# Kernel optimization log

Hardware: AMD Instinct MI355X
Metric: run time of the kernel (lower is better)

The kernel has to match this reference:

```python
import jax, jax.numpy as jnp
import numpy as np

D = 256       # dim
M = 50        # num_celltypes
NPATH = 65536 # path tokens (256*256)
N = M + NPATH
FF = 3        # focusing_factor
K = 5         # dwc kernel size


def find_closest_factors(num):
    for i in range(int(num ** 0.5), 0, -1):
        if num % i == 0:
            return (i, num // i)
    return (1, num)


def setup_inputs() -> dict:
    key = jax.random.key(0)
    ks = jax.random.split(key, 16)
    def w(k, shape, s=0.02):
        return jax.random.normal(k, shape, dtype=jnp.float32) * s
    z = lambda *s: jnp.zeros(s, jnp.float32)
    return {
        "x": jax.random.normal(ks[0], (1, N, D), dtype=jnp.float32),
        "W_qkv": w(ks[1], (D, 3 * D)),
        "scale_linear": w(ks[2], (1, 1, D)),
        "dwc_w": w(ks[3], (D, 1, K, K)),
        "dwc_b": w(ks[4], (D,)),
        "Wa": w(ks[5], (D, D)), "ba": z(D),
        "Wb": w(ks[6], (D, D)), "bb": z(D),
        "Wc": w(ks[7], (D, 1)), "bc": z(1),
        "W1": w(ks[8], (D, D)), "b1": z(D),
        "W2": w(ks[9], (D, D)), "b2": z(D),
        "W3a": w(ks[10], (2 * D, D)), "b3a": z(D),
        "W3b": w(ks[11], (D, D)), "b3b": z(D),
        "Wf": w(ks[12], (D, D)), "bf": z(D),
    }


def reference(x, W_qkv, scale_linear, dwc_w, dwc_b, Wa, ba, Wb, bb, Wc, bc,
              W1, b1, W2, b2, W3a, b3a, W3b, b3b, Wf, bf):
    scale = D ** -0.5
    qkv = x @ W_qkv                         # (1, N, 3D)
    q, k, v = jnp.split(qkv, 3, axis=-1)
    qc, qp = q[:, :M], q[:, M:]
    kc, kp = k[:, :M], k[:, M:]
    vc, vp = v[:, :M], v[:, M:]

    # --- softmax attention branches ---
    sa = jax.nn.softmax(jnp.einsum('bic,bjc->bij', qc * scale, kc), axis=-1)
    out_self_celltypes = sa @ vc            # (1, M, D)
    cap = jax.nn.softmax(jnp.einsum('bic,bjc->bij', qp * scale, kc), axis=-1)
    out_cross_path = cap @ vc               # (1, NPATH, D)
    cac = jax.nn.softmax(jnp.einsum('bic,bjc->bij', qc * scale, kp), axis=-1)
    out_cross_celltypes = cac @ vp          # (1, M, D)

    # --- focused linear attention on path tokens ---
    sp = jax.nn.softplus(scale_linear)
    ql = (jax.nn.relu(qp) + 1e-6) / sp
    kl = (jax.nn.relu(kp) + 1e-6) / sp
    qn = jnp.linalg.norm(ql, axis=-1, keepdims=True)
    kn = jnp.linalg.norm(kl, axis=-1, keepdims=True)
    ql = ql ** FF
    kl = kl ** FF
    ql = ql / jnp.linalg.norm(ql, axis=-1, keepdims=True) * qn
    kl = kl / jnp.linalg.norm(kl, axis=-1, keepdims=True) * kn
    zfac = 1.0 / (jnp.einsum('bic,bc->bi', ql, kl.sum(axis=1)) + 1e-6)
    kv = jnp.einsum('bjc,bjd->bcd', kl, vp)                 # (1, D, D)
    out_s = jnp.einsum('bic,bcd,bi->bid', ql, kv, zfac)     # (1, NPATH, D)

    # --- depthwise conv feature map ---
    wc, hc = find_closest_factors(NPATH)
    fm = vp.reshape(1, wc, hc, D).transpose(0, 3, 1, 2)     # b c w h
    fm = jax.lax.conv_general_dilated(
        fm, dwc_w, (1, 1), 'SAME',
        dimension_numbers=('NCHW', 'OIHW', 'NCHW'), feature_group_count=D)
    fm = fm + dwc_b[None, :, None, None]
    fm = fm.transpose(0, 2, 3, 1).reshape(1, NPATH, D)
    out_self_path = (out_s + fm) @ Wf + bf  # feamap_linear (dropout=eval)

    # --- gated attention net (shared weights, 4 calls) ---
    def gated(t):
        t = t[0]  # squeeze batch -> (n, D)
        a = jnp.tanh(t @ Wa + ba)
        g = jax.nn.sigmoid(t @ Wb + bb)
        return (a * g) @ Wc + bc  # (n, 1)

    A_cc = gated(out_cross_celltypes)
    A_cp = gated(out_cross_path)
    A_sc = gated(out_self_celltypes)
    A_sp = gated(out_self_path)

    # --- attention fusion (shared weights, 2 calls) ---
    def fuse(A1, A2, x1, x2):
        h1 = jax.nn.softmax(A1.T, axis=1) @ x1[0]   # (1, D)
        h1 = jax.nn.relu(h1 @ W1 + b1)
        h2 = jax.nn.softmax(A2.T, axis=1) @ x2[0]
        h2 = jax.nn.relu(h2 @ W2 + b2)
        f = jnp.concatenate([h1, h2], axis=1)       # (1, 2D)
        return jax.nn.relu(jax.nn.relu(f @ W3a + b3a) @ W3b + b3b)

    fusion_cross = fuse(A_cc, A_cp, out_cross_celltypes, out_cross_path)
    fusion_self = fuse(A_sc, A_sp, out_self_celltypes, out_self_path)
    return jnp.concatenate([fusion_cross, fusion_self], axis=1)  # (1, 2D)
```

## Files before the change

kernel.cpp:

```cpp
#include <hip/hip_runtime.h>
#include <hip/hip_bf16.h>
#include <math.h>


constexpr int DD = 256;
constexpr int MM = 50;
constexpr float SCL = 0.0625f;

constexpr size_t B_VPH = 0;
constexpr size_t B_QLH = (size_t)32 << 20;
constexpr size_t B_KLH = (size_t)64 << 20;
constexpr size_t B_E   = (size_t)96 << 20;
constexpr size_t B_SM  = (size_t)112 << 20;
constexpr size_t B_X   = B_SM + ((size_t)2 << 20);

constexpr size_t PP_OFF = (size_t)4 << 20;

constexpr size_t KLSUMR = 0;
constexpr size_t KLSUMP = 256;
constexpr size_t OCCDENP= 2304;
constexpr size_t W50P   = 2816;
constexpr size_t EDENP  = 3328;
constexpr size_t H2TP   = 3336;
constexpr size_t H2DENP = 5384;
constexpr size_t OCCRAW = 5392;
constexpr size_t ZEND   = 18192;
constexpr size_t QC     = ZEND;
constexpr size_t KC     = QC + 12800;
constexpr size_t VC     = KC + 12800;
constexpr size_t VCA    = VC + 12800;
constexpr size_t VCB    = VCA + 12800;
constexpr size_t WFA    = VCB + 12800;
constexpr size_t WFB    = WFA + 65536;
constexpr size_t BFA    = WFB + 65536;
constexpr size_t BFB    = BFA + 256;
constexpr size_t OSCB   = BFB + 256;
constexpr size_t OCCB   = OSCB + 12800;
constexpr size_t ASC    = OCCB + 12800;
constexpr size_t ACC50  = ASC + 64;
constexpr size_t SMEND  = ACC50 + 64;

constexpr size_t XT_WQKV = 0;
constexpr size_t XT_WFAT = 196608;
constexpr size_t XT_WFBT = 262144;
constexpr size_t XT_KVT  = 327680;
constexpr size_t XT_QCH  = 393216;
constexpr size_t XT_KCH  = 409600;
constexpr size_t XT_VCAT = 425984;
constexpr size_t XT_VCBT = 442368;
constexpr size_t XT_END  = 458752;
constexpr size_t WS_NEEDED = B_X + XT_END * 2;

typedef short bf16x8 __attribute__((ext_vector_type(8)));
typedef float f32x4 __attribute__((ext_vector_type(4)));

__device__ __forceinline__ float rcpf_(float x){ return __builtin_amdgcn_rcpf(x); }
__device__ __forceinline__ float fsig_(float x){ return rcpf_(1.0f + __expf(-x)); }
__device__ __forceinline__ float ftanh_(float x){ return 1.0f - 2.0f * rcpf_(__expf(2.0f * x) + 1.0f); }

__device__ __forceinline__ float bf2f(unsigned short u){
  return __uint_as_float(((unsigned int)u) << 16);
}
__device__ __forceinline__ unsigned short f2bf(float f){
  union { __hip_bfloat16 h; unsigned short u; } c;
  c.h = __float2bfloat16(f);
  return c.u;
}
__device__ __forceinline__ f32x4 mfma16(bf16x8 a, bf16x8 b, f32x4 c){
  return __builtin_amdgcn_mfma_f32_16x16x32_bf16(a, b, c, 0, 0, 0);
}

__device__ __forceinline__ float waveAllSum(float v){
  #pragma unroll
  for (int m = 1; m < 64; m <<= 1) v += __shfl_xor(v, m, 64);
  return v;
}

__device__ __forceinline__ size_t fragIdx(int n, int k, int K8){
  const int tile = n >> 4, cn = n & 15;
  const int k0 = k >> 5, kqi = (k >> 3) & 3, e = k & 7;
  return (((size_t)tile * K8 + k0) * 64 + (kqi * 16 + cn)) * 8 + e;
}

__device__ __forceinline__ int kvOff(int c, int k){
  return c * 40 + (c >> 3) * 8 + k;
}

__global__ void __launch_bounds__(256) k_prep0(const float* __restrict__ x, const float* __restrict__ Wqkv,
                                               float* qc, float* kc, float* vc,
                                               unsigned short* qch, unsigned short* kch,
                                               unsigned short* __restrict__ WT,
                                               const float* __restrict__ Wa, const float* __restrict__ Wb,
                                               const float* __restrict__ ba, const float* __restrict__ bb,
                                               const float* __restrict__ Wf, const float* __restrict__ bf,
                                               float* Wfa, float* Wfb, float* bfa, float* bfb,
                                               unsigned short* WfaTh, unsigned short* WfbTh){
  const int b = blockIdx.x, t = threadIdx.x;
  if (b < 48) {
    __shared__ unsigned short Tt[64][72];
    const int bn = b % 12, bk = b / 12;
    const int n0 = bn * 64, k0g = bk * 64;
    #pragma unroll
    for (int i = 0; i < 16; i++) {
      const int k_l = (t >> 6) + i * 4;
      const int n_l = t & 63;
      Tt[n_l][k_l] = f2bf(Wqkv[(size_t)(k0g + k_l) * 768 + n0 + n_l]);
    }
    __syncthreads();
    #pragma unroll
    for (int i = 0; i < 2; i++) {
      const int fr = t * 2 + i;
      const int t_l = fr >> 7;
      const int k0_l = (fr >> 6) & 1;
      const int lane_f = fr & 63;
      const int n_l = t_l * 16 + (lane_f & 15);
      const int k_l = k0_l * 32 + (lane_f >> 4) * 8;
      const int tg = (n0 >> 4) + t_l;
      const int k0gl = (k0g >> 5) + k0_l;
      bf16x8 v = *(const bf16x8*)&Tt[n_l][k_l];
      *(bf16x8*)&WT[(((size_t)tg * 8 + k0gl) * 64 + lane_f) * 8] = v;
    }
    return;
  }
  __shared__ float xs[256];
  const int j = t;
  if (b < 98) {
    const int r = b - 48;
    xs[j] = x[r * DD + j];
    __syncthreads();
    float aq = 0.f, ak = 0.f, av = 0.f;
    for (int k = 0; k < DD; k++) {
      float xv = xs[k];
      aq += xv * Wqkv[k * 768 + j];
      ak += xv * Wqkv[k * 768 + 256 + j];
      av += xv * Wqkv[k * 768 + 512 + j];
    }
    qc[r * DD + j] = aq; kc[r * DD + j] = ak; vc[r * DD + j] = av;
    qch[fragIdx(r, j, 8)] = f2bf(aq);
    kch[fragIdx(r, j, 8)] = f2bf(ak);
    if (r == 0) {
      for (int c = 50; c < 64; c++) {
        qch[fragIdx(c, j, 8)] = 0;
        kch[fragIdx(c, j, 8)] = 0;
      }
    }
    return;
  }
  const int bb2 = b - 98;
  const float* src; const float* Wm;
  if (bb2 < 256)      { src = Wf + bb2 * DD;         Wm = Wa; }
  else if (bb2 < 512) { src = Wf + (bb2 - 256) * DD; Wm = Wb; }
  else if (bb2 == 512){ src = bf;                    Wm = Wa; }
  else                { src = bf;                    Wm = Wb; }
  xs[j] = src[j];
  __syncthreads();
  float a = 0.f;
  for (int k = 0; k < DD; k++) a += xs[k] * Wm[k * DD + j];
  if (bb2 < 256)      { Wfa[bb2 * DD + j] = a; WfaTh[fragIdx(j, bb2, 8)] = f2bf(a); }
  else if (bb2 < 512) { Wfb[(bb2 - 256) * DD + j] = a; WfbTh[fragIdx(j, bb2 - 256, 8)] = f2bf(a); }
  else if (bb2 == 512) bfa[j] = a + ba[j];
  else bfb[j] = a + bb[j];
}

__global__ void __launch_bounds__(256) k_prep1(const float* vc, const float* Wa, const float* Wb,
                                               float* Vca, float* Vcb,
                                               unsigned short* VcaTh, unsigned short* VcbTh){
  __shared__ float rs[256];
  const int b = blockIdx.x, j = threadIdx.x;
  const int r = b;
  rs[j] = vc[r * DD + j];
  __syncthreads();
  float a = 0.f, bv = 0.f;
  for (int k = 0; k < DD; k++) { float v = rs[k]; a += v * Wa[k * DD + j]; bv += v * Wb[k * DD + j]; }
  Vca[r * DD + j] = a; Vcb[r * DD + j] = bv;
  VcaTh[fragIdx(j, r, 2)] = f2bf(a);
  VcbTh[fragIdx(j, r, 2)] = f2bf(bv);
  if (r == 0) {
    for (int c = 50; c < 64; c++) {
      VcaTh[fragIdx(j, c, 2)] = 0;
      VcbTh[fragIdx(j, c, 2)] = 0;
    }
  }
}

__global__ void __launch_bounds__(256) k_oscg(const float* __restrict__ qc, const float* __restrict__ kc,
                                              const float* __restrict__ vc,
                                              const float* __restrict__ Wa, const float* __restrict__ Wb,
                                              const float* __restrict__ ba, const float* __restrict__ bb,
                                              const float* __restrict__ Wc, const float* __restrict__ bc,
                                              float* __restrict__ osc, float* __restrict__ A){
  const int i = blockIdx.x, t = threadIdx.x;
  __shared__ float qs[256];
  __shared__ float P[64];
  __shared__ float red[4];
  qs[t] = qc[i * DD + t];
  __syncthreads();
  if (t < 64) {
    float s = -1e30f;
    if (t < 50) {
      float acc = 0.f;
      const float4* kr = (const float4*)&kc[t * DD];
      #pragma unroll 8
      for (int k = 0; k < 64; k++) {
        float4 kv = kr[k];
        float4 qv = *(const float4*)&qs[k * 4];
        acc += qv.x * kv.x + qv.y * kv.y + qv.z * kv.z + qv.w * kv.w;
      }
      s = acc * SCL;
    }
    float mx = s;
    #pragma unroll
    for (int m = 1; m < 64; m <<= 1) mx = fmaxf(mx, __shfl_xor(mx, m, 64));
    float e = (t < 50) ? __expf(s - mx) : 0.f;
    float den = waveAllSum(e);
    P[t] = e * rcpf_(den);
  }
  __syncthreads();
  float a = 0.f;
  for (int jj = 0; jj < 50; jj++) a += P[jj] * vc[jj * DD + t];
  osc[i * DD + t] = a;
  __syncthreads();
  qs[t] = a;
  __syncthreads();
  float u = 0.f, v = 0.f;
  for (int k = 0; k < DD; k++) { float tv = qs[k]; u += tv * Wa[k * DD + t]; v += tv * Wb[k * DD + t]; }
  float g = ftanh_(u + ba[t]) * fsig_(v + bb[t]) * Wc[t];
  g = waveAllSum(g);
  const int lane = t & 63, wv = t >> 6;
  if (lane == 0) red[wv] = g;
  __syncthreads();
  if (t == 0) A[i] = red[0] + red[1] + red[2] + red[3] + bc[0];
}

__global__ void __launch_bounds__(256) k_path1(
    const float* __restrict__ x, const unsigned short* __restrict__ WTf,
    const float* __restrict__ sln,
    const unsigned short* __restrict__ kchf, const unsigned short* __restrict__ qchf,
    const unsigned short* __restrict__ VcaTf, const unsigned short* __restrict__ VcbTf,
    const float* __restrict__ ba, const float* __restrict__ bb,
    const float* __restrict__ Wc, const float* __restrict__ bc,
    unsigned short* __restrict__ vph, unsigned short* __restrict__ qlh, unsigned short* __restrict__ klh,
    unsigned short* __restrict__ Eh, float* __restrict__ w50p, float* __restrict__ edenp, float* __restrict__ occdenp){
  __shared__ __align__(16) char arena[38912];
  unsigned short (*Psh)[72]   = (unsigned short (*)[72])arena;
  float (*denp)[4]            = (float (*)[4])(arena + 4608);
  unsigned short (*qpsb)[264] = (unsigned short (*)[264])(arena + 5120);
  unsigned short (*kpsb)[264] = (unsigned short (*)[264])(arena + 22016);

  const int tid = threadIdx.x;
  const int i0 = blockIdx.x * 32;
  const int part = blockIdx.x & 7;
  const int lane = tid & 63;
  const int wvv = tid >> 6;
  const int cn = lane & 15;
  const int m0 = (lane >> 4) * 4;
  const int kq = (lane >> 4) * 8;

  for (int l = tid; l < 2048; l += 256) {
    const int r = l >> 6, c4 = (l & 63) * 4;
    const float4 xv = *(const float4*)&x[(size_t)(MM + i0 + r) * DD + c4];
    ushort4 o; o.x = f2bf(xv.x); o.y = f2bf(xv.y); o.z = f2bf(xv.z); o.w = f2bf(xv.w);
    *(ushort4*)&qpsb[r][c4] = o;
  }
  __syncthreads();

  bf16x8 af0[8], af1[8];
  #pragma unroll
  for (int k0 = 0; k0 < 8; k0++) {
    af0[k0] = *(const bf16x8*)&qpsb[cn][k0 * 32 + kq];
    af1[k0] = *(const bf16x8*)&qpsb[16 + cn][k0 * 32 + kq];
  }
  __syncthreads();

  bf16x8 b0[8], b1[8];
  {
    const unsigned short* Bt = WTf + ((size_t)wvv * 8 * 64 + lane) * 8;
    #pragma unroll
    for (int k0 = 0; k0 < 8; k0++) b0[k0] = *(const bf16x8*)&Bt[(size_t)k0 * 512];
  }
  #pragma unroll 1
  for (int tt = 0; tt < 12; tt++) {
    const int t = wvv + 4 * tt;
    if (tt + 1 < 12) {
      const unsigned short* Bt = WTf + (((size_t)(t + 4) * 8) * 64 + lane) * 8;
      #pragma unroll
      for (int k0 = 0; k0 < 8; k0++) b1[k0] = *(const bf16x8*)&Bt[(size_t)k0 * 512];
    }
    f32x4 acc0 = {0.f, 0.f, 0.f, 0.f};
    f32x4 acc1 = {0.f, 0.f, 0.f, 0.f};
    #pragma unroll
    for (int k0 = 0; k0 < 8; k0++) {
      acc0 = mfma16(af0[k0], b0[k0], acc0);
      acc1 = mfma16(af1[k0], b0[k0], acc1);
    }
    if (t < 16) {
      int c = t * 16 + cn;
      #pragma unroll
      for (int i = 0; i < 4; i++) {
        qpsb[m0 + i][c] = f2bf(acc0[i]);
        qpsb[16 + m0 + i][c] = f2bf(acc1[i]);
      }
    } else if (t < 32) {
      int c = (t - 16) * 16 + cn;
      #pragma unroll
      for (int i = 0; i < 4; i++) {
        kpsb[m0 + i][c] = f2bf(acc0[i]);
        kpsb[16 + m0 + i][c] = f2bf(acc1[i]);
      }
    } else {
      int c = (t - 32) * 16 + cn;
      #pragma unroll
      for (int i = 0; i < 4; i++) {
        vph[(size_t)(i0 + m0 + i) * DD + c] = f2bf(acc0[i]);
        vph[(size_t)(i0 + 16 + m0 + i) * DD + c] = f2bf(acc1[i]);
      }
    }
    #pragma unroll
    for (int k0 = 0; k0 < 8; k0++) b0[k0] = b1[k0];
  }
  __syncthreads();

  float ep0[4], ep1[4];
  {
    f32x4 accp0 = {0.f,0.f,0.f,0.f}, accp1 = {0.f,0.f,0.f,0.f};
    f32x4 accc0 = {0.f,0.f,0.f,0.f}, accc1 = {0.f,0.f,0.f,0.f};
    const unsigned short* Bk = kchf + ((size_t)wvv * 8 * 64 + lane) * 8;
    const unsigned short* Bq = qchf + ((size_t)wvv * 8 * 64 + lane) * 8;
    #pragma unroll
    for (int k0 = 0; k0 < 8; k0++) {
      bf16x8 aq0 = *(const bf16x8*)&qpsb[cn][k0 * 32 + kq];
      bf16x8 aq1 = *(const bf16x8*)&qpsb[16 + cn][k0 * 32 + kq];
      bf16x8 ak0 = *(const bf16x8*)&kpsb[cn][k0 * 32 + kq];
      bf16x8 ak1 = *(const bf16x8*)&kpsb[16 + cn][k0 * 32 + kq];
      bf16x8 bk = *(const bf16x8*)&Bk[(size_t)k0 * 512];
      bf16x8 bq = *(const bf16x8*)&Bq[(size_t)k0 * 512];
      accp0 = mfma16(aq0, bk, accp0);
      accp1 = mfma16(aq1, bk, accp1);
      accc0 = mfma16(ak0, bq, accc0);
      accc1 = mfma16(ak1, bq, accc1);
    }
    const int col = wvv * 16 + cn;
    const bool ok = (col < 50);
    #pragma unroll
    for (int i = 0; i < 4; i++) {
      ep0[i] = ok ? __expf(accp0[i] * SCL) : 0.f;
      ep1[i] = ok ? __expf(accp1[i] * SCL) : 0.f;
    }
    float osum = 0.f;
    #pragma unroll
    for (int i = 0; i < 4; i++) {
      unsigned short h0 = ok ? f2bf(__expf(accc0[i] * SCL)) : (unsigned short)0;
      unsigned short h1 = ok ? f2bf(__expf(accc1[i] * SCL)) : (unsigned short)0;
      Eh[(size_t)(i0 + m0 + i) * 64 + col] = h0;
      Eh[(size_t)(i0 + 16 + m0 + i) * 64 + col] = h1;
      if (ok) osum += bf2f(h0) + bf2f(h1);
    }
    osum += __shfl_xor(osum, 16, 64);
    osum += __shfl_xor(osum, 32, 64);
    if (lane < 16 && ok) atomicAdd(&occdenp[part * 64 + col], osum);
    float d0[4], d1[4];
    #pragma unroll
    for (int i = 0; i < 4; i++) { d0[i] = ep0[i]; d1[i] = ep1[i]; }
    #pragma unroll
    for (int m = 1; m < 16; m <<= 1) {
      #pragma unroll
      for (int i = 0; i < 4; i++) {
        d0[i] += __shfl_xor(d0[i], m, 64);
        d1[i] += __shfl_xor(d1[i], m, 64);
      }
    }
    if (cn == 0) {
      #pragma unroll
      for (int i = 0; i < 4; i++) {
        denp[m0 + i][wvv] = d0[i];
        denp[16 + m0 + i][wvv] = d1[i];
      }
    }
  }
  __syncthreads();

  {
    const int col = wvv * 16 + cn;
    #pragma unroll
    for (int i = 0; i < 4; i++) {
      float4 dp = *(const float4*)&denp[m0 + i][0];
      Psh[m0 + i][col] = f2bf(ep0[i] * rcpf_(dp.x + dp.y + dp.z + dp.w));
      float4 dq = *(const float4*)&denp[16 + m0 + i][0];
      Psh[16 + m0 + i][col] = f2bf(ep1[i] * rcpf_(dq.x + dq.y + dq.z + dq.w));
    }
  }

  float4 sl4 = ((const float4*)sln)[lane];
  float4 rsp;
  rsp.x = rcpf_(log1pf(expf(sl4.x))); rsp.y = rcpf_(log1pf(expf(sl4.y)));
  rsp.z = rcpf_(log1pf(expf(sl4.z))); rsp.w = rcpf_(log1pf(expf(sl4.w)));
  float4 ba4 = ((const float4*)ba)[lane];
  float4 bb4 = ((const float4*)bb)[lane];
  float4 wc4 = ((const float4*)Wc)[lane];
  float bcv = bc[0];
  for (int rr = 0; rr < 8; rr++) {
    const int r = wvv * 8 + rr;
    const int row = i0 + r;
    ushort4 qu = *(const ushort4*)&qpsb[r][lane * 4];
    ushort4 ku = *(const ushort4*)&kpsb[r][lane * 4];
    float4 q4 = {bf2f(qu.x), bf2f(qu.y), bf2f(qu.z), bf2f(qu.w)};
    float4 k4 = {bf2f(ku.x), bf2f(ku.y), bf2f(ku.z), bf2f(ku.w)};
    float4 lq, lk;
    lq.x = (fmaxf(q4.x, 0.f) + 1e-6f) * rsp.x; lq.y = (fmaxf(q4.y, 0.f) + 1e-6f) * rsp.y;
    lq.z = (fmaxf(q4.z, 0.f) + 1e-6f) * rsp.z; lq.w = (fmaxf(q4.w, 0.f) + 1e-6f) * rsp.w;
    lk.x = (fmaxf(k4.x, 0.f) + 1e-6f) * rsp.x; lk.y = (fmaxf(k4.y, 0.f) + 1e-6f) * rsp.y;
    lk.z = (fmaxf(k4.z, 0.f) + 1e-6f) * rsp.z; lk.w = (fmaxf(k4.w, 0.f) + 1e-6f) * rsp.w;
    float4 q3, k3;
    q3.x = lq.x*lq.x*lq.x; q3.y = lq.y*lq.y*lq.y; q3.z = lq.z*lq.z*lq.z; q3.w = lq.w*lq.w*lq.w;
    k3.x = lk.x*lk.x*lk.x; k3.y = lk.y*lk.y*lk.y; k3.z = lk.z*lk.z*lk.z; k3.w = lk.w*lk.w*lk.w;
    float n1q = lq.x*lq.x + lq.y*lq.y + lq.z*lq.z + lq.w*lq.w;
    float n3q = q3.x*q3.x + q3.y*q3.y + q3.z*q3.z + q3.w*q3.w;
    float n1k = lk.x*lk.x + lk.y*lk.y + lk.z*lk.z + lk.w*lk.w;
    float n3k = k3.x*k3.x + k3.y*k3.y + k3.z*k3.z + k3.w*k3.w;
    n1q = waveAllSum(n1q); n3q = waveAllSum(n3q);
    n1k = waveAllSum(n1k); n3k = waveAllSum(n3k);
    float fq = sqrtf(n1q * rcpf_(n3q));
    float fk = sqrtf(n1k * rcpf_(n3k));
    ushort4 qo, ko;
    qo.x = f2bf(q3.x * fq); qo.y = f2bf(q3.y * fq); qo.z = f2bf(q3.z * fq); qo.w = f2bf(q3.w * fq);
    ko.x = f2bf(k3.x * fk); ko.y = f2bf(k3.y * fk); ko.z = f2bf(k3.z * fk); ko.w = f2bf(k3.w * fk);
    *(ushort4*)&qlh[(size_t)row * DD + lane * 4] = qo;
    *(ushort4*)&klh[(size_t)row * DD + lane * 4] = ko;
  }
  __syncthreads();

  {
    bf16x8 ap0[2], ap1[2];
    #pragma unroll
    for (int k0 = 0; k0 < 2; k0++) {
      ap0[k0] = *(const bf16x8*)&Psh[cn][k0 * 32 + kq];
      ap1[k0] = *(const bf16x8*)&Psh[16 + cn][k0 * 32 + kq];
    }
    #pragma unroll 1
    for (int tt = 0; tt < 4; tt++) {
      const int nt = wvv * 4 + tt;
      const unsigned short* Bu = VcaTf + (((size_t)nt * 2) * 64 + lane) * 8;
      const unsigned short* Bv = VcbTf + (((size_t)nt * 2) * 64 + lane) * 8;
      f32x4 au0 = {0.f,0.f,0.f,0.f}, au1 = {0.f,0.f,0.f,0.f};
      f32x4 av0 = {0.f,0.f,0.f,0.f}, av1 = {0.f,0.f,0.f,0.f};
      #pragma unroll
      for (int k0 = 0; k0 < 2; k0++) {
        bf16x8 bu = *(const bf16x8*)&Bu[(size_t)k0 * 512];
        bf16x8 bv = *(const bf16x8*)&Bv[(size_t)k0 * 512];
        au0 = mfma16(ap0[k0], bu, au0);
        au1 = mfma16(ap1[k0], bu, au1);
        av0 = mfma16(ap0[k0], bv, av0);
        av1 = mfma16(ap1[k0], bv, av1);
      }
      #pragma unroll
      for (int i = 0; i < 4; i++) {
        qpsb[m0 + i][nt * 16 + cn] = f2bf(au0[i]);
        qpsb[16 + m0 + i][nt * 16 + cn] = f2bf(au1[i]);
        kpsb[m0 + i][nt * 16 + cn] = f2bf(av0[i]);
        kpsb[16 + m0 + i][nt * 16 + cn] = f2bf(av1[i]);
      }
    }
  }
  __syncthreads();

  #pragma unroll
  for (int rr = 0; rr < 8; rr++) {
    const int r = wvv * 8 + rr;
    ushort4 uu = *(const ushort4*)&qpsb[r][lane * 4];
    ushort4 vv = *(const ushort4*)&kpsb[r][lane * 4];
    float g = ftanh_(bf2f(uu.x) + ba4.x) * fsig_(bf2f(vv.x) + bb4.x) * wc4.x
            + ftanh_(bf2f(uu.y) + ba4.y) * fsig_(bf2f(vv.y) + bb4.y) * wc4.y
            + ftanh_(bf2f(uu.z) + ba4.z) * fsig_(bf2f(vv.z) + bb4.z) * wc4.z
            + ftanh_(bf2f(uu.w) + ba4.w) * fsig_(bf2f(vv.w) + bb4.w) * wc4.w;
    g = waveAllSum(g);
    if (lane == 0) *(float*)&Psh[r][64] = __expf(g + bcv);
  }
  __syncthreads();
  if (tid < 64) {
    float s = 0.f;
    #pragma unroll
    for (int r = 0; r < 32; r++) s += *(const float*)&Psh[r][64] * bf2f(Psh[r][tid]);
    atomicAdd(&w50p[part * 64 + tid], s);
  }
  if (tid == 0) {
    float es = 0.f;
    #pragma unroll
    for (int r = 0; r < 32; r++) es += *(const float*)&Psh[r][64];
    atomicAdd(&edenp[part], es);
  }
}

__global__ void __launch_bounds__(256) k_kv(const unsigned short* __restrict__ klh,
                                            const unsigned short* __restrict__ Eh,
                                            const unsigned short* __restrict__ vph,
                                            unsigned short* __restrict__ PP,
                                            float* __restrict__ klsump,
                                            float* __restrict__ occraw){
  __shared__ __align__(16) unsigned short AT[2608];
  __shared__ __align__(16) unsigned short BvpT[10480];
  const int tid = threadIdx.x;
  const int lane = tid & 63;
  const int wvv = tid >> 6;
  const int cn = lane & 15;
  const int m0 = (lane >> 4) * 4;
  const int kq = (lane >> 4) * 8;
  const int cb = blockIdx.x;
  const int z  = blockIdx.y;
  const int jj = tid >> 3;
  const int c8 = (tid & 7) * 8;
  const bool isOcc = (cb == 4);

  f32x4 acc[4][4];
  f32x4 acc1[4];
  #pragma unroll
  for (int mt = 0; mt < 4; mt++) {
    acc1[mt] = (f32x4){0.f,0.f,0.f,0.f};
    #pragma unroll
    for (int tl = 0; tl < 4; tl++) acc[mt][tl] = (f32x4){0.f,0.f,0.f,0.f};
  }
  bf16x8 ones;
  #pragma unroll
  for (int i = 0; i < 8; i++) ones[i] = (short)0x3F80;

  const int jbase = z * 1024;
  #pragma unroll 1
  for (int step = 0; step < 32; step++) {
    const int j0 = jbase + step * 32;
    {
      bf16x8 av;
      if (isOcc) av = *(const bf16x8*)&Eh[(size_t)(j0 + jj) * 64 + c8];
      else       av = *(const bf16x8*)&klh[(size_t)(j0 + jj) * 256 + cb * 64 + c8];
      #pragma unroll
      for (int i = 0; i < 8; i++) AT[kvOff(c8 + i, jj)] = (unsigned short)av[i];
      #pragma unroll
      for (int rep = 0; rep < 4; rep++) {
        bf16x8 bv = *(const bf16x8*)&vph[(size_t)(j0 + jj) * 256 + rep * 64 + c8];
        #pragma unroll
        for (int i = 0; i < 8; i++) BvpT[kvOff(rep * 64 + c8 + i, jj)] = (unsigned short)bv[i];
      }
    }
    __syncthreads();
    bf16x8 afr[4], bfr[4];
    #pragma unroll
    for (int mt = 0; mt < 4; mt++)
      afr[mt] = *(const bf16x8*)&AT[kvOff(cn + mt * 16, kq)];
    #pragma unroll
    for (int tl = 0; tl < 4; tl++)
      bfr[tl] = *(const bf16x8*)&BvpT[kvOff(wvv * 64 + tl * 16 + cn, kq)];
    if (!isOcc) {
      #pragma unroll
      for (int mt = 0; mt < 4; mt++) acc1[mt] = mfma16(afr[mt], ones, acc1[mt]);
    }
    #pragma unroll
    for (int mt = 0; mt < 4; mt++)
      #pragma unroll
      for (int tl = 0; tl < 4; tl++) acc[mt][tl] = mfma16(afr[mt], bfr[tl], acc[mt][tl]);
    __syncthreads();
  }
  if (isOcc) {
    #pragma unroll
    for (int mt = 0; mt < 4; mt++)
      #pragma unroll
      for (int i = 0; i < 4; i++) {
        const int ri = mt * 16 + m0 + i;
        if (ri < 50) {
          #pragma unroll
          for (int tl = 0; tl < 4; tl++) {
            const int d = wvv * 64 + tl * 16 + cn;
            atomicAdd(&occraw[ri * DD + d], acc[mt][tl][i]);
          }
        }
      }
    return;
  }
  unsigned short* P = PP + ((size_t)(cb * 64 + z)) * 16384;
  #pragma unroll
  for (int mt = 0; mt < 4; mt++)
    #pragma unroll
    for (int tl = 0; tl < 4; tl++) {
      const int n = (wvv * 4 + tl) * 16 + cn;
      #pragma unroll
      for (int i = 0; i < 4; i++)
        P[(size_t)(mt * 16 + m0 + i) * 256 + n] = f2bf(acc[mt][tl][i]);
    }
  if (wvv == 0 && cn == 0) {
    #pragma unroll
    for (int mt = 0; mt < 4; mt++)
      #pragma unroll
      for (int i = 0; i < 4; i++)
        atomicAdd(&klsump[(z & 7) * 256 + cb * 64 + mt * 16 + m0 + i], acc1[mt][i]);
  }
}

__global__ void __launch_bounds__(256) k_fin2(const unsigned short* __restrict__ PP,
                                              unsigned short* __restrict__ kvTf,
                                              const float* __restrict__ occraw,
                                              const float* __restrict__ occdenp,
                                              float* __restrict__ occ,
                                              const float* __restrict__ klsump,
                                              float* __restrict__ klsum,
                                              const float* __restrict__ Wa, const float* __restrict__ Wb,
                                              const float* __restrict__ ba, const float* __restrict__ bb,
                                              const float* __restrict__ Wc, const float* __restrict__ bc,
                                              float* __restrict__ A){
  __shared__ float ts[256];
  __shared__ float red[4];
  const int b = blockIdx.x, tid = threadIdx.x;
  if (b < 32) {
    const int gm = b * 8 + (tid >> 5);
    const int cb = gm >> 6, m = gm & 63;
    const int d8 = (tid & 31) * 8;
    float s[8];
    #pragma unroll
    for (int e = 0; e < 8; e++) s[e] = 0.f;
    for (int z = 0; z < 64; z++) {
      bf16x8 v = *(const bf16x8*)&PP[((size_t)(cb * 64 + z)) * 16384 + (size_t)m * 256 + d8];
      #pragma unroll
      for (int e = 0; e < 8; e++) s[e] += bf2f((unsigned short)v[e]);
    }
    #pragma unroll
    for (int e = 0; e < 8; e++)
      kvTf[fragIdx(d8 + e, gm, 8)] = f2bf(s[e]);
  } else if (b < 82) {
    const int i = b - 32, j = tid;
    float den = 0.f;
    #pragma unroll
    for (int p = 0; p < 8; p++) den += occdenp[p * 64 + i];
    float t = occraw[i * DD + j] / den;
    occ[i * DD + j] = t;
    ts[j] = t;
    __syncthreads();
    float u = 0.f, v = 0.f;
    for (int k = 0; k < DD; k++) { float tv = ts[k]; u += tv * Wa[k * DD + j]; v += tv * Wb[k * DD + j]; }
    float g = ftanh_(u + ba[j]) * fsig_(v + bb[j]) * Wc[j];
    g = waveAllSum(g);
    const int lane = j & 63, wv = j >> 6;
    if (lane == 0) red[wv] = g;
    __syncthreads();
    if (j == 0) A[i] = red[0] + red[1] + red[2] + red[3] + bc[0];
  } else {
    const int d = tid;
    float s = 0.f;
    #pragma unroll
    for (int p = 0; p < 8; p++) s += klsump[p * 256 + d];
    klsum[d] = s;
  }
}

__global__ void __launch_bounds__(256) k_tail(const unsigned short* __restrict__ qlh,
                                              const unsigned short* __restrict__ kvTf,
                                              const float* __restrict__ klsum,
                                              const unsigned short* __restrict__ vph,
                                              const float* __restrict__ dwcw, const float* __restrict__ dwcb,
                                              const unsigned short* __restrict__ WfaTf,
                                              const unsigned short* __restrict__ WfbTf,
                                              const float* __restrict__ bfa, const float* __restrict__ bfb,
                                              const float* __restrict__ Wc, const float* __restrict__ bc,
                                              float* __restrict__ h2tp, float* __restrict__ h2denp){
  __shared__ unsigned short Tsh[32][264];
  __shared__ unsigned short OSb[32][264];
  __shared__ unsigned short aVb[32][264];
  __shared__ float zf[32];
  __shared__ float ev[32];
  const int tid = threadIdx.x;
  const int i0 = blockIdx.x * 32;
  const int part = blockIdx.x & 7;
  const int lane = tid & 63;
  const int wvv = tid >> 6;
  const int cn = lane & 15;
  const int m0 = (lane >> 4) * 4;
  const int kq = (lane >> 4) * 8;
  for (int l = tid; l < 2048; l += 256) {
    int r = l >> 6, c4 = (l & 63) * 4;
    *(ushort4*)&Tsh[r][c4] = *(const ushort4*)&qlh[(size_t)(i0 + r) * DD + c4];
  }
  __syncthreads();
  {
    bf16x8 afq0[8], afq1[8];
    #pragma unroll
    for (int k0 = 0; k0 < 8; k0++) {
      afq0[k0] = *(const bf16x8*)&Tsh[cn][k0 * 32 + kq];
      afq1[k0] = *(const bf16x8*)&Tsh[16 + cn][k0 * 32 + kq];
    }
    #pragma unroll 1
    for (int tt = 0; tt < 4; tt++) {
      const int nt = wvv * 4 + tt;
      const unsigned short* Bt = kvTf + (((size_t)nt * 8) * 64 + lane) * 8;
      f32x4 acc0 = {0.f,0.f,0.f,0.f};
      f32x4 acc1 = {0.f,0.f,0.f,0.f};
      #pragma unroll
      for (int k0 = 0; k0 < 8; k0++) {
        bf16x8 b = *(const bf16x8*)&Bt[(size_t)k0 * 512];
        acc0 = mfma16(afq0[k0], b, acc0);
        acc1 = mfma16(afq1[k0], b, acc1);
      }
      #pragma unroll
      for (int i = 0; i < 4; i++) {
        OSb[m0 + i][nt * 16 + cn] = f2bf(acc0[i]);
        OSb[16 + m0 + i][nt * 16 + cn] = f2bf(acc1[i]);
      }
    }
  }
  {
    float4 ks4 = ((const float4*)klsum)[lane];
    #pragma unroll
    for (int rr = 0; rr < 8; rr++) {
      const int r = wvv * 8 + rr;
      ushort4 q4 = *(const ushort4*)&Tsh[r][lane * 4];
      float s = bf2f(q4.x)*ks4.x + bf2f(q4.y)*ks4.y + bf2f(q4.z)*ks4.z + bf2f(q4.w)*ks4.w;
      s = waveAllSum(s);
      if (lane == 0) zf[r] = rcpf_(s + 1e-6f);
    }
  }
  __syncthreads();
  const int j = tid;
  float w[25];
  #pragma unroll
  for (int t = 0; t < 25; t++) w[t] = dwcw[j * 25 + t];
  const float bias = dwcb[j];
  const int y = i0 >> 8, x0 = i0 & 255;
  float fm[32];
  #pragma unroll
  for (int r = 0; r < 32; r++) fm[r] = bias;
  #pragma unroll
  for (int dy = -2; dy <= 2; dy++) {
    const int yy = y + dy;
    if ((unsigned)yy > 255u) continue;
    float buf[36];
    #pragma unroll
    for (int i = 0; i < 36; i++) {
      const int xx = x0 - 2 + i;
      buf[i] = ((unsigned)xx <= 255u) ? bf2f(vph[(size_t)((yy << 8) + xx) * DD + j]) : 0.f;
    }
    const float* wr = &w[(dy + 2) * 5];
    #pragma unroll
    for (int r = 0; r < 32; r++)
      fm[r] += buf[r] * wr[0] + buf[r+1] * wr[1] + buf[r+2] * wr[2]
             + buf[r+3] * wr[3] + buf[r+4] * wr[4];
  }
  #pragma unroll
  for (int r = 0; r < 32; r++) {
    fm[r] = bf2f(OSb[r][j]) * zf[r] + fm[r];
    Tsh[r][j] = f2bf(fm[r]);
  }
  __syncthreads();
  {
    bf16x8 aft0[8], aft1[8];
    #pragma unroll
    for (int k0 = 0; k0 < 8; k0++) {
      aft0[k0] = *(const bf16x8*)&Tsh[cn][k0 * 32 + kq];
      aft1[k0] = *(const bf16x8*)&Tsh[16 + cn][k0 * 32 + kq];
    }
    #pragma unroll 1
    for (int jb = 0; jb < 8; jb++) {
      const int nt = wvv * 4 + (jb & 3);
      const unsigned short* Bt = ((jb < 4) ? WfaTf : WfbTf) + (((size_t)nt * 8) * 64 + lane) * 8;
      f32x4 acc0 = {0.f,0.f,0.f,0.f};
      f32x4 acc1 = {0.f,0.f,0.f,0.f};
      #pragma unroll
      for (int k0 = 0; k0 < 8; k0++) {
        bf16x8 b = *(const bf16x8*)&Bt[(size_t)k0 * 512];
        acc0 = mfma16(aft0[k0], b, acc0);
        acc1 = mfma16(aft1[k0], b, acc1);
      }
      unsigned short (*dst)[264] = (jb < 4) ? OSb : aVb;
      #pragma unroll
      for (int i = 0; i < 4; i++) {
        dst[m0 + i][nt * 16 + cn] = f2bf(acc0[i]);
        dst[16 + m0 + i][nt * 16 + cn] = f2bf(acc1[i]);
      }
    }
  }
  __syncthreads();
  {
    float4 bfa4 = ((const float4*)bfa)[lane];
    float4 bfb4 = ((const float4*)bfb)[lane];
    float4 wc4 = ((const float4*)Wc)[lane];
    const float bcv = bc[0];
    #pragma unroll
    for (int rr = 0; rr < 8; rr++) {
      const int r = wvv * 8 + rr;
      ushort4 uu = *(const ushort4*)&OSb[r][lane * 4];
      ushort4 vv = *(const ushort4*)&aVb[r][lane * 4];
      float g = ftanh_(bf2f(uu.x) + bfa4.x) * fsig_(bf2f(vv.x) + bfb4.x) * wc4.x
              + ftanh_(bf2f(uu.y) + bfa4.y) * fsig_(bf2f(vv.y) + bfb4.y) * wc4.y
              + ftanh_(bf2f(uu.z) + bfa4.z) * fsig_(bf2f(vv.z) + bfb4.z) * wc4.z
              + ftanh_(bf2f(uu.w) + bfa4.w) * fsig_(bf2f(vv.w) + bfb4.w) * wc4.w;
      g = waveAllSum(g);
      if (lane == 0) ev[r] = __expf(g + bcv);
    }
  }
  __syncthreads();
  float hp = 0.f;
  #pragma unroll
  for (int r = 0; r < 32; r++) hp += ev[r] * fm[r];
  atomicAdd(&h2tp[part * 256 + j], hp);
  if (tid == 0) {
    float es = 0.f;
    #pragma unroll
    for (int r = 0; r < 32; r++) es += ev[r];
    atomicAdd(&h2denp[part], es);
  }
}

__global__ void __launch_bounds__(256) k_final(
    const float* __restrict__ A_cc, const float* __restrict__ occ,
    const float* __restrict__ A_sc, const float* __restrict__ osc,
    const float* __restrict__ w50p, const float* __restrict__ edenp,
    const float* __restrict__ h2tp, const float* __restrict__ h2denp,
    const float* __restrict__ vc, const float* __restrict__ Wf, const float* __restrict__ bf,
    const float* __restrict__ W1, const float* __restrict__ b1,
    const float* __restrict__ W2, const float* __restrict__ b2,
    const float* __restrict__ W3a, const float* __restrict__ b3a,
    const float* __restrict__ W3b, const float* __restrict__ b3b,
    float* __restrict__ out){
  int j = threadIdx.x;
  __shared__ float pw[64];
  __shared__ float w50t[64];
  __shared__ float t1[256], t2[256], h1[256], h2[256], fz[512], z1[256];
  if (j < 64) {
    float s = 0.f;
    #pragma unroll
    for (int p = 0; p < 8; p++) s += w50p[p * 64 + j];
    w50t[j] = s;
  }
  float edentot = 0.f, h2dentot = 0.f;
  #pragma unroll
  for (int p = 0; p < 8; p++) { edentot += edenp[p]; h2dentot += h2denp[p]; }
  if (j < 64) pw[j] = (j < 50) ? expf(A_cc[j]) : 0.f;
  __syncthreads();
  float den = 0.f;
  for (int i = 0; i < 50; i++) den += pw[i];
  float raw = 0.f;
  for (int i = 0; i < 50; i++) raw += pw[i] * occ[i * DD + j];
  t1[j] = raw / den;
  float r2 = 0.f;
  for (int i = 0; i < 50; i++) r2 += w50t[i] * vc[i * DD + j];
  t2[j] = r2 / edentot;
  __syncthreads();
  float a1 = 0.f, a2 = 0.f;
  for (int k = 0; k < DD; k++) { a1 += t1[k] * W1[k * DD + j]; a2 += t2[k] * W2[k * DD + j]; }
  h1[j] = fmaxf(a1 + b1[j], 0.f);
  h2[j] = fmaxf(a2 + b2[j], 0.f);
  __syncthreads();
  fz[j] = h1[j]; fz[256 + j] = h2[j];
  __syncthreads();
  float z = 0.f;
  for (int k = 0; k < 512; k++) z += fz[k] * W3a[k * DD + j];
  z1[j] = fmaxf(z + b3a[j], 0.f);
  __syncthreads();
  float o = 0.f;
  for (int k = 0; k < DD; k++) o += z1[k] * W3b[k * DD + j];
  out[j] = fmaxf(o + b3b[j], 0.f);
  __syncthreads();
  if (j < 64) pw[j] = (j < 50) ? expf(A_sc[j]) : 0.f;
  __syncthreads();
  den = 0.f;
  for (int i = 0; i < 50; i++) den += pw[i];
  raw = 0.f;
  for (int i = 0; i < 50; i++) raw += pw[i] * osc[i * DD + j];
  t1[j] = raw / den;
  {
    float s = 0.f;
    #pragma unroll
    for (int p = 0; p < 8; p++) s += h2tp[p * 256 + j];
    t2[j] = s / h2dentot;
  }
  __syncthreads();
  float hs = 0.f;
  for (int k = 0; k < DD; k++) hs += t2[k] * Wf[k * DD + j];
  __syncthreads();
  t2[j] = hs + bf[j];
  __syncthreads();
  a1 = 0.f; a2 = 0.f;
  for (int k = 0; k < DD; k++) { a1 += t1[k] * W1[k * DD + j]; a2 += t2[k] * W2[k * DD + j]; }
  h1[j] = fmaxf(a1 + b1[j], 0.f);
  h2[j] = fmaxf(a2 + b2[j], 0.f);
  __syncthreads();
  fz[j] = h1[j]; fz[256 + j] = h2[j];
  __syncthreads();
  z = 0.f;
  for (int k = 0; k < 512; k++) z += fz[k] * W3a[k * DD + j];
  z1[j] = fmaxf(z + b3a[j], 0.f);
  __syncthreads();
  o = 0.f;
  for (int k = 0; k < DD; k++) o += z1[k] * W3b[k * DD + j];
  out[256 + j] = fmaxf(o + b3b[j], 0.f);
}

extern "C" void kernel_launch(void* const* d_in, const int* in_sizes, int n_in,
                              void* d_out, int out_size, void* d_ws, size_t ws_size,
                              hipStream_t stream) {
  if (ws_size < WS_NEEDED) return;
  const float* x   = (const float*)d_in[0];
  const float* Wqkv= (const float*)d_in[1];
  const float* sln = (const float*)d_in[2];
  const float* dwcw= (const float*)d_in[3];
  const float* dwcb= (const float*)d_in[4];
  const float* Wa  = (const float*)d_in[5];
  const float* ba  = (const float*)d_in[6];
  const float* Wb  = (const float*)d_in[7];
  const float* bb  = (const float*)d_in[8];
  const float* Wc  = (const float*)d_in[9];
  const float* bc  = (const float*)d_in[10];
  const float* W1  = (const float*)d_in[11];
  const float* b1  = (const float*)d_in[12];
  const float* W2  = (const float*)d_in[13];
  const float* b2  = (const float*)d_in[14];
  const float* W3a = (const float*)d_in[15];
  const float* b3a = (const float*)d_in[16];
  const float* W3b = (const float*)d_in[17];
  const float* b3b = (const float*)d_in[18];
  const float* Wf  = (const float*)d_in[19];
  const float* bf  = (const float*)d_in[20];

  char* wsb = (char*)d_ws;
  unsigned short* VPH = (unsigned short*)(wsb + B_VPH);
  unsigned short* QLH = (unsigned short*)(wsb + B_QLH);
  unsigned short* KLH = (unsigned short*)(wsb + B_KLH);
  unsigned short* EHB = (unsigned short*)(wsb + B_E);
  unsigned short* PPB = EHB + PP_OFF;
  float* SM = (float*)(wsb + B_SM);
  unsigned short* XT = (unsigned short*)(wsb + B_X);
  float* outp = (float*)d_out;

  hipMemsetAsync((void*)SM, 0, ZEND * sizeof(float), stream);

  k_prep0<<<612, 256, 0, stream>>>(x, Wqkv, SM + QC, SM + KC, SM + VC,
                                   XT + XT_QCH, XT + XT_KCH, XT + XT_WQKV,
                                   Wa, Wb, ba, bb, Wf, bf,
                                   SM + WFA, SM + WFB, SM + BFA, SM + BFB,
                                   XT + XT_WFAT, XT + XT_WFBT);
  k_prep1<<<50, 256, 0, stream>>>(SM + VC, Wa, Wb,
                                  SM + VCA, SM + VCB, XT + XT_VCAT, XT + XT_VCBT);
  k_oscg<<<50, 256, 0, stream>>>(SM + QC, SM + KC, SM + VC, Wa, Wb, ba, bb, Wc, bc,
                                 SM + OSCB, SM + ASC);

  k_path1<<<2048, 256, 0, stream>>>(x, XT + XT_WQKV, sln, XT + XT_KCH, XT + XT_QCH,
                                    XT + XT_VCAT, XT + XT_VCBT, ba, bb, Wc, bc,
                                    VPH, QLH, KLH, EHB, SM + W50P, SM + EDENP, SM + OCCDENP);
  k_kv<<<dim3(5, 64), 256, 0, stream>>>(KLH, EHB, VPH, PPB, SM + KLSUMP, SM + OCCRAW);
  k_fin2<<<83, 256, 0, stream>>>(PPB, XT + XT_KVT,
                                 SM + OCCRAW, SM + OCCDENP, SM + OCCB,
                                 SM + KLSUMP, SM + KLSUMR,
                                 Wa, Wb, ba, bb, Wc, bc, SM + ACC50);

  k_tail<<<2048, 256, 0, stream>>>(QLH, XT + XT_KVT, SM + KLSUMR, VPH, dwcw, dwcb,
                                   XT + XT_WFAT, XT + XT_WFBT, SM + BFA, SM + BFB,
                                   Wc, bc, SM + H2TP, SM + H2DENP);

  k_final<<<1, 256, 0, stream>>>(SM + ACC50, SM + OCCB, SM + ASC, SM + OSCB,
                                 SM + W50P, SM + EDENP, SM + H2TP, SM + H2DENP,
                                 SM + VC, Wf, bf, W1, b1, W2, b2, W3a, b3a, W3b, b3b, outp);
}
```

Before: 512.8 us.

## Merge prep kernels, double-buffer k_kv LDS tiles, split final fusion across two blocks

Three separate changes. k_prep1 and k_oscg become one 100-block launch, which removes a kernel launch and lets the two independent jobs run at the same time. k_kv gets double-buffered shared-memory tiles: each step loads the next tile's global data into registers, runs the MFMAs on the current buffer, then writes the next buffer, so there is one barrier per step instead of two. k_final now runs its two independent fusion branches on two blocks in parallel instead of one after the other. In exchange, k_kv needs twice the LDS and more registers, which may lower occupancy.

```diff
diff --git a/kernel.cpp b/kernel.cpp
--- a/kernel.cpp
+++ b/kernel.cpp
@@ -162,34 +162,34 @@
   else bfb[j] = a + bb[j];
 }
 
-__global__ void __launch_bounds__(256) k_prep1(const float* vc, const float* Wa, const float* Wb,
-                                               float* Vca, float* Vcb,
-                                               unsigned short* VcaTh, unsigned short* VcbTh){
-  __shared__ float rs[256];
-  const int b = blockIdx.x, j = threadIdx.x;
-  const int r = b;
-  rs[j] = vc[r * DD + j];
-  __syncthreads();
-  float a = 0.f, bv = 0.f;
-  for (int k = 0; k < DD; k++) { float v = rs[k]; a += v * Wa[k * DD + j]; bv += v * Wb[k * DD + j]; }
-  Vca[r * DD + j] = a; Vcb[r * DD + j] = bv;
-  VcaTh[fragIdx(j, r, 2)] = f2bf(a);
-  VcbTh[fragIdx(j, r, 2)] = f2bf(bv);
-  if (r == 0) {
-    for (int c = 50; c < 64; c++) {
-      VcaTh[fragIdx(j, c, 2)] = 0;
-      VcbTh[fragIdx(j, c, 2)] = 0;
-    }
-  }
-}
-
-__global__ void __launch_bounds__(256) k_oscg(const float* __restrict__ qc, const float* __restrict__ kc,
-                                              const float* __restrict__ vc,
-                                              const float* __restrict__ Wa, const float* __restrict__ Wb,
-                                              const float* __restrict__ ba, const float* __restrict__ bb,
-                                              const float* __restrict__ Wc, const float* __restrict__ bc,
-                                              float* __restrict__ osc, float* __restrict__ A){
-  const int i = blockIdx.x, t = threadIdx.x;
+__global__ void __launch_bounds__(256) k_prep1g(const float* __restrict__ vc,
+                                                const float* __restrict__ qc, const float* __restrict__ kc,
+                                                const float* __restrict__ Wa, const float* __restrict__ Wb,
+                                                const float* __restrict__ ba, const float* __restrict__ bb,
+                                                const float* __restrict__ Wc, const float* __restrict__ bc,
+                                                float* Vca, float* Vcb,
+                                                unsigned short* VcaTh, unsigned short* VcbTh,
+                                                float* __restrict__ osc, float* __restrict__ A){
+  const int b = blockIdx.x, t = threadIdx.x;
+  if (b < 50) {
+    __shared__ float rs[256];
+    const int r = b, j = t;
+    rs[j] = vc[r * DD + j];
+    __syncthreads();
+    float a = 0.f, bv = 0.f;
+    for (int k = 0; k < DD; k++) { float v = rs[k]; a += v * Wa[k * DD + j]; bv += v * Wb[k * DD + j]; }
+    Vca[r * DD + j] = a; Vcb[r * DD + j] = bv;
+    VcaTh[fragIdx(j, r, 2)] = f2bf(a);
+    VcbTh[fragIdx(j, r, 2)] = f2bf(bv);
+    if (r == 0) {
+      for (int c = 50; c < 64; c++) {
+        VcaTh[fragIdx(j, c, 2)] = 0;
+        VcbTh[fragIdx(j, c, 2)] = 0;
+      }
+    }
+    return;
+  }
+  const int i = b - 50;
   __shared__ float qs[256];
   __shared__ float P[64];
   __shared__ float red[4];
@@ -496,8 +496,8 @@
                                             unsigned short* __restrict__ PP,
                                             float* __restrict__ klsump,
                                             float* __restrict__ occraw){
-  __shared__ __align__(16) unsigned short AT[2608];
-  __shared__ __align__(16) unsigned short BvpT[10480];
+  __shared__ __align__(16) unsigned short AT[2][2608];
+  __shared__ __align__(16) unsigned short BvpT[2][10480];
   const int tid = threadIdx.x;
   const int lane = tid & 63;
   const int wvv = tid >> 6;
@@ -523,38 +523,58 @@
   for (int i = 0; i < 8; i++) ones[i] = (short)0x3F80;
 
   const int jbase = z * 1024;
+  {
+    const int j0 = jbase;
+    bf16x8 av;
+    if (isOcc) av = *(const bf16x8*)&Eh[(size_t)(j0 + jj) * 64 + c8];
+    else       av = *(const bf16x8*)&klh[(size_t)(j0 + jj) * 256 + cb * 64 + c8];
+    #pragma unroll
+    for (int i = 0; i < 8; i++) AT[0][kvOff(c8 + i, jj)] = (unsigned short)av[i];
+    #pragma unroll
+    for (int rep = 0; rep < 4; rep++) {
+      bf16x8 bv = *(const bf16x8*)&vph[(size_t)(j0 + jj) * 256 + rep * 64 + c8];
+      #pragma unroll
+      for (int i = 0; i < 8; i++) BvpT[0][kvOff(rep * 64 + c8 + i, jj)] = (unsigned short)bv[i];
+    }
+  }
+  __syncthreads();
+
   #pragma unroll 1
   for (int step = 0; step < 32; step++) {
-    const int j0 = jbase + step * 32;
-    {
-      bf16x8 av;
-      if (isOcc) av = *(const bf16x8*)&Eh[(size_t)(j0 + jj) * 64 + c8];
-      else       av = *(const bf16x8*)&klh[(size_t)(j0 + jj) * 256 + cb * 64 + c8];
-      #pragma unroll
-      for (int i = 0; i < 8; i++) AT[kvOff(c8 + i, jj)] = (unsigned short)av[i];
-      #pragma unroll
-      for (int rep = 0; rep < 4; rep++) {
-        bf16x8 bv = *(const bf16x8*)&vph[(size_t)(j0 + jj) * 256 + rep * 64 + c8];
+    const int cur = step & 1;
+    bf16x8 avn, bvn[4];
+    if (step + 1 < 32) {
+      const int j0 = jbase + (step + 1) * 32;
+      if (isOcc) avn = *(const bf16x8*)&Eh[(size_t)(j0 + jj) * 64 + c8];
+      else       avn = *(const bf16x8*)&klh[(size_t)(j0 + jj) * 256 + cb * 64 + c8];
+      #pragma unroll
+      for (int rep = 0; rep < 4; rep++)
+        bvn[rep] = *(const bf16x8*)&vph[(size_t)(j0 + jj) * 256 + rep * 64 + c8];
+    }
+    bf16x8 afr[4], bfr[4];
+    #pragma unroll
+    for (int mt = 0; mt < 4; mt++)
+      afr[mt] = *(const bf16x8*)&AT[cur][kvOff(cn + mt * 16, kq)];
+    #pragma unroll
+    for (int tl = 0; tl < 4; tl++)
+      bfr[tl] = *(const bf16x8*)&BvpT[cur][kvOff(wvv * 64 + tl * 16 + cn, kq)];
+    if (!isOcc) {
+      #pragma unroll
+      for (int mt = 0; mt < 4; mt++) acc1[mt] = mfma16(afr[mt], ones, acc1[mt]);
+    }
+    #pragma unroll
+    for (int mt = 0; mt < 4; mt++)
+      #pragma unroll
+      for (int tl = 0; tl < 4; tl++) acc[mt][tl] = mfma16(afr[mt], bfr[tl], acc[mt][tl]);
+    if (step + 1 < 32) {
+      const int nb = cur ^ 1;
+      #pragma unroll
+      for (int i = 0; i < 8; i++) AT[nb][kvOff(c8 + i, jj)] = (unsigned short)avn[i];
+      #pragma unroll
+      for (int rep = 0; rep < 4; rep++)
         #pragma unroll
-        for (int i = 0; i < 8; i++) BvpT[kvOff(rep * 64 + c8 + i, jj)] = (unsigned short)bv[i];
-      }
-    }
-    __syncthreads();
-    bf16x8 afr[4], bfr[4];
-    #pragma unroll
-    for (int mt = 0; mt < 4; mt++)
-      afr[mt] = *(const bf16x8*)&AT[kvOff(cn + mt * 16, kq)];
-    #pragma unroll
-    for (int tl = 0; tl < 4; tl++)
-      bfr[tl] = *(const bf16x8*)&BvpT[kvOff(wvv * 64 + tl * 16 + cn, kq)];
-    if (!isOcc) {
-      #pragma unroll
-      for (int mt = 0; mt < 4; mt++) acc1[mt] = mfma16(afr[mt], ones, acc1[mt]);
-    }
-    #pragma unroll
-    for (int mt = 0; mt < 4; mt++)
-      #pragma unroll
-      for (int tl = 0; tl < 4; tl++) acc[mt][tl] = mfma16(afr[mt], bfr[tl], acc[mt][tl]);
+        for (int i = 0; i < 8; i++) BvpT[nb][kvOff(rep * 64 + c8 + i, jj)] = (unsigned short)bvn[rep][i];
+    }
     __syncthreads();
   }
   if (isOcc) {
@@ -817,75 +837,75 @@
   int j = threadIdx.x;
   __shared__ float pw[64];
   __shared__ float w50t[64];
-  __shared__ float t1[256], t2[256], h1[256], h2[256], fz[512], z1[256];
-  if (j < 64) {
-    float s = 0.f;
-    #pragma unroll
-    for (int p = 0; p < 8; p++) s += w50p[p * 64 + j];
-    w50t[j] = s;
-  }
-  float edentot = 0.f, h2dentot = 0.f;
-  #pragma unroll
-  for (int p = 0; p < 8; p++) { edentot += edenp[p]; h2dentot += h2denp[p]; }
-  if (j < 64) pw[j] = (j < 50) ? expf(A_cc[j]) : 0.f;
-  __syncthreads();
-  float den = 0.f;
-  for (int i = 0; i < 50; i++) den += pw[i];
-  float raw = 0.f;
-  for (int i = 0; i < 50; i++) raw += pw[i] * occ[i * DD + j];
-  t1[j] = raw / den;
-  float r2 = 0.f;
-  for (int i = 0; i < 50; i++) r2 += w50t[i] * vc[i * DD + j];
-  t2[j] = r2 / edentot;
-  __syncthreads();
-  float a1 = 0.f, a2 = 0.f;
-  for (int k = 0; k < DD; k++) { a1 += t1[k] * W1[k * DD + j]; a2 += t2[k] * W2[k * DD + j]; }
-  h1[j] = fmaxf(a1 + b1[j], 0.f);
-  h2[j] = fmaxf(a2 + b2[j], 0.f);
-  __syncthreads();
-  fz[j] = h1[j]; fz[256 + j] = h2[j];
-  __syncthreads();
-  float z = 0.f;
-  for (int k = 0; k < 512; k++) z += fz[k] * W3a[k * DD + j];
-  z1[j] = fmaxf(z + b3a[j], 0.f);
-  __syncthreads();
-  float o = 0.f;
-  for (int k = 0; k < DD; k++) o += z1[k] * W3b[k * DD + j];
-  out[j] = fmaxf(o + b3b[j], 0.f);
-  __syncthreads();
-  if (j < 64) pw[j] = (j < 50) ? expf(A_sc[j]) : 0.f;
-  __syncthreads();
-  den = 0.f;
-  for (int i = 0; i < 50; i++) den += pw[i];
-  raw = 0.f;
-  for (int i = 0; i < 50; i++) raw += pw[i] * osc[i * DD + j];
-  t1[j] = raw / den;
-  {
-    float s = 0.f;
-    #pragma unroll
-    for (int p = 0; p < 8; p++) s += h2tp[p * 256 + j];
-    t2[j] = s / h2dentot;
-  }
-  __syncthreads();
-  float hs = 0.f;
-  for (int k = 0; k < DD; k++) hs += t2[k] * Wf[k * DD + j];
-  __syncthreads();
-  t2[j] = hs + bf[j];
-  __syncthreads();
-  a1 = 0.f; a2 = 0.f;
-  for (int k = 0; k < DD; k++) { a1 += t1[k] * W1[k * DD + j]; a2 += t2[k] * W2[k * DD + j]; }
-  h1[j] = fmaxf(a1 + b1[j], 0.f);
-  h2[j] = fmaxf(a2 + b2[j], 0.f);
-  __syncthreads();
-  fz[j] = h1[j]; fz[256 + j] = h2[j];
-  __syncthreads();
-  z = 0.f;
-  for (int k = 0; k < 512; k++) z += fz[k] * W3a[k * DD + j];
-  z1[j] = fmaxf(z + b3a[j], 0.f);
-  __syncthreads();
-  o = 0.f;
-  for (int k = 0; k < DD; k++) o += z1[k] * W3b[k * DD + j];
-  out[256 + j] = fmaxf(o + b3b[j], 0.f);
+  __shared__ float t1[256], t2[256], fz[512], z1[256];
+  if (blockIdx.x == 0) {
+    if (j < 64) {
+      float s = 0.f;
+      #pragma unroll
+      for (int p = 0; p < 8; p++) s += w50p[p * 64 + j];
+      w50t[j] = s;
+    }
+    float edentot = 0.f;
+    #pragma unroll
+    for (int p = 0; p < 8; p++) edentot += edenp[p];
+    if (j < 64) pw[j] = (j < 50) ? expf(A_cc[j]) : 0.f;
+    __syncthreads();
+    float den = 0.f;
+    for (int i = 0; i < 50; i++) den += pw[i];
+    float raw = 0.f;
+    for (int i = 0; i < 50; i++) raw += pw[i] * occ[i * DD + j];
+    t1[j] = raw / den;
+    float r2 = 0.f;
+    for (int i = 0; i < 50; i++) r2 += w50t[i] * vc[i * DD + j];
+    t2[j] = r2 / edentot;
+    __syncthreads();
+    float a1 = 0.f, a2 = 0.f;
+    for (int k = 0; k < DD; k++) { a1 += t1[k] * W1[k * DD + j]; a2 += t2[k] * W2[k * DD + j]; }
+    fz[j] = fmaxf(a1 + b1[j], 0.f);
+    fz[256 + j] = fmaxf(a2 + b2[j], 0.f);
+    __syncthreads();
+    float z = 0.f;
+    for (int k = 0; k < 512; k++) z += fz[k] * W3a[k * DD + j];
+    z1[j] = fmaxf(z + b3a[j], 0.f);
+    __syncthreads();
+    float o = 0.f;
+    for (int k = 0; k < DD; k++) o += z1[k] * W3b[k * DD + j];
+    out[j] = fmaxf(o + b3b[j], 0.f);
+  } else {
+    float h2dentot = 0.f;
+    #pragma unroll
+    for (int p = 0; p < 8; p++) h2dentot += h2denp[p];
+    if (j < 64) pw[j] = (j < 50) ? expf(A_sc[j]) : 0.f;
+    {
+      float s = 0.f;
+      #pragma unroll
+      for (int p = 0; p < 8; p++) s += h2tp[p * 256 + j];
+      t2[j] = s / h2dentot;
+    }
+    __syncthreads();
+    float den = 0.f;
+    for (int i = 0; i < 50; i++) den += pw[i];
+    float raw = 0.f;
+    for (int i = 0; i < 50; i++) raw += pw[i] * osc[i * DD + j];
+    t1[j] = raw / den;
+    float hs = 0.f;
+    for (int k = 0; k < DD; k++) hs += t2[k] * Wf[k * DD + j];
+    __syncthreads();
+    t2[j] = hs + bf[j];
+    __syncthreads();
+    float a1 = 0.f, a2 = 0.f;
+    for (int k = 0; k < DD; k++) { a1 += t1[k] * W1[k * DD + j]; a2 += t2[k] * W2[k * DD + j]; }
+    fz[j] = fmaxf(a1 + b1[j], 0.f);
+    fz[256 + j] = fmaxf(a2 + b2[j], 0.f);
+    __syncthreads();
+    float z = 0.f;
+    for (int k = 0; k < 512; k++) z += fz[k] * W3a[k * DD + j];
+    z1[j] = fmaxf(z + b3a[j], 0.f);
+    __syncthreads();
+    float o = 0.f;
+    for (int k = 0; k < DD; k++) o += z1[k] * W3b[k * DD + j];
+    out[256 + j] = fmaxf(o + b3b[j], 0.f);
+  }
 }
 
 extern "C" void kernel_launch(void* const* d_in, const int* in_sizes, int n_in,
@@ -931,10 +951,10 @@
                                    Wa, Wb, ba, bb, Wf, bf,
                                    SM + WFA, SM + WFB, SM + BFA, SM + BFB,
                                    XT + XT_WFAT, XT + XT_WFBT);
-  k_prep1<<<50, 256, 0, stream>>>(SM + VC, Wa, Wb,
-                                  SM + VCA, SM + VCB, XT + XT_VCAT, XT + XT_VCBT);
-  k_oscg<<<50, 256, 0, stream>>>(SM + QC, SM + KC, SM + VC, Wa, Wb, ba, bb, Wc, bc,
-                                 SM + OSCB, SM + ASC);
+  k_prep1g<<<100, 256, 0, stream>>>(SM + VC, SM + QC, SM + KC,
+                                    Wa, Wb, ba, bb, Wc, bc,
+                                    SM + VCA, SM + VCB, XT + XT_VCAT, XT + XT_VCBT,
+                                    SM + OSCB, SM + ASC);
 
   k_path1<<<2048, 256, 0, stream>>>(x, XT + XT_WQKV, sln, XT + XT_KCH, XT + XT_QCH,
                                     XT + XT_VCAT, XT + XT_VCBT, ba, bb, Wc, bc,
@@ -949,7 +969,7 @@
                                    XT + XT_WFAT, XT + XT_WFBT, SM + BFA, SM + BFB,
                                    Wc, bc, SM + H2TP, SM + H2DENP);
 
-  k_final<<<1, 256, 0, stream>>>(SM + ACC50, SM + OCCB, SM + ASC, SM + OSCB,
+  k_final<<<2, 256, 0, stream>>>(SM + ACC50, SM + OCCB, SM + ASC, SM + OSCB,
                                  SM + W50P, SM + EDENP, SM + H2TP, SM + H2DENP,
                                  SM + VC, Wf, bf, W1, b1, W2, b2, W3a, b3a, W3b, b3b, outp);
 }
```

After: 470.1 us (median of 2 runs). 8.3% less time.
